# Kernel tuning notes

Measured on AMD Instinct MI355X. Metric: run time of the kernel, lower is better.

## Reference

```python
import jax, jax.numpy as jnp
import numpy as np

B, V, K, C = 32, 65536, 8, 3


def setup_inputs() -> dict:
    key = jax.random.key(0)
    k1, k2, k3, k4 = jax.random.split(key, 4)
    out = jax.random.normal(k1, (B, V, C), dtype=jnp.float32)
    tgt = jax.random.normal(k2, (B, V, C), dtype=jnp.float32)
    neighbor_idxs = jax.random.randint(k3, (V, K), 0, V, dtype=jnp.int32)
    # Laplacian weights: each row sums to -1 (lap = x - weighted mean of neighbors)
    w = jax.random.uniform(k4, (V, K), dtype=jnp.float32) + 1e-3
    neighbor_weights = -w / jnp.sum(w, axis=-1, keepdims=True)
    return {
        "out": out,
        "tgt": tgt,
        "neighbor_idxs": neighbor_idxs,
        "neighbor_weights": neighbor_weights,
    }


def _compute_laplacian(x, neighbor_idxs, neighbor_weights):
    # x: [B, V, C]; gather -> [B, V, K, C]; weighted sum over K; residual add
    gathered = x[:, neighbor_idxs]                       # [B, V, K, C]
    return x + jnp.sum(gathered * neighbor_weights[None, :, :, None], axis=2)


def reference(out, tgt, neighbor_idxs, neighbor_weights):
    lap_out = _compute_laplacian(out, neighbor_idxs, neighbor_weights)
    lap_tgt = _compute_laplacian(tgt, neighbor_idxs, neighbor_weights)
    return (lap_out - lap_tgt) ** 2
```

## Files before the change

### kernel.cpp

```cpp
#include <hip/hip_runtime.h>

#define BB 32
#define VV 65536
#define KK 8
#define CC 3

constexpr int TV   = 64;
constexpr int ROW  = BB * CC;
constexpr int PROW = ROW + 1;
constexpr int TILE_ELEMS = TV * ROW;
constexpr int ROWU = ROW / 2;

__device__ __forceinline__ unsigned int f2bf(float f) {
  unsigned int u = __float_as_uint(f);
  u += 0x7FFFu + ((u >> 16) & 1u);
  return u >> 16;
}
__device__ __forceinline__ float bflo(unsigned int u) { return __uint_as_float(u << 16); }
__device__ __forceinline__ float bfhi(unsigned int u) { return __uint_as_float(u & 0xFFFF0000u); }

__global__ __launch_bounds__(256) void lap_pass1_transpose_sub(
    const float* __restrict__ outp, const float* __restrict__ tgtp,
    unsigned int* __restrict__ dt) {
  __shared__ float tile[TV * PROW];
  const int t  = threadIdx.x;
  const int v0 = blockIdx.x * TV;

  const float4* o4 = (const float4*)outp;
  const float4* t4 = (const float4*)tgtp;
  const int src_base4 = (v0 * CC) >> 2;
  #pragma unroll
  for (int l4 = t; l4 < TILE_ELEMS / 4; l4 += 256) {
    int b  = l4 / (TV * CC / 4);
    int j4 = l4 - b * (TV * CC / 4);
    int src = b * (VV * CC / 4) + src_base4 + j4;
    float4 a = o4[src];
    float4 g = t4[src];
    float dv[4] = {a.x - g.x, a.y - g.y, a.z - g.z, a.w - g.w};
    int j = 4 * j4;
    #pragma unroll
    for (int q = 0; q < 4; q++) {
      int jj = j + q;
      int vrel = jj / CC, c = jj - vrel * CC;
      tile[vrel * PROW + b * CC + c] = dv[q];
    }
  }
  __syncthreads();

  uint4* dst = (uint4*)(dt + (size_t)v0 * ROWU);
  #pragma unroll
  for (int i8 = t; i8 < TILE_ELEMS / 8; i8 += 256) {
    int e = i8 * 8;
    int vrel = e / ROW, r = e - vrel * ROW;
    const float* p = &tile[vrel * PROW + r];
    uint4 o;
    o.x = f2bf(p[0]) | (f2bf(p[1]) << 16);
    o.y = f2bf(p[2]) | (f2bf(p[3]) << 16);
    o.z = f2bf(p[4]) | (f2bf(p[5]) << 16);
    o.w = f2bf(p[6]) | (f2bf(p[7]) << 16);
    dst[i8] = o;
  }
}

__global__ __launch_bounds__(256) void lap_pass2_gather(
    const unsigned int* __restrict__ dt, const int* __restrict__ nidx,
    const float* __restrict__ nw, float* __restrict__ res) {
  __shared__ float rtile[TV * PROW];
  __shared__ int   idx_s[TV * KK];
  __shared__ float w_s[TV * KK];
  const int t  = threadIdx.x;
  const int v0 = blockIdx.x * TV;

  for (int l = t; l < TV * KK; l += 256) {
    idx_s[l] = nidx[v0 * KK + l];
    w_s[l]   = nw[v0 * KK + l];
  }
  __syncthreads();

  const int g = t >> 4;
  const int l = t & 15;
  #pragma unroll 2
  for (int i = 0; i < TV / 16; i++) {
    const int vrel = i * 16 + g;
    const int v    = v0 + vrel;

    const int4*   ip = (const int4*)&idx_s[vrel * KK];
    const float4* wp = (const float4*)&w_s[vrel * KK];
    int4   ia = ip[0], ib = ip[1];
    float4 wa = wp[0], wb = wp[1];
    int   nbk[KK] = {ia.x, ia.y, ia.z, ia.w, ib.x, ib.y, ib.z, ib.w};
    float wk[KK]  = {wa.x, wa.y, wa.z, wa.w, wb.x, wb.y, wb.z, wb.w};

    const unsigned int* sp = dt + (size_t)v * ROWU + 3 * l;
    unsigned int s0 = sp[0], s1 = sp[1], s2 = sp[2];
    float x0 = bflo(s0), y0 = bfhi(s0), z0 = bflo(s1);
    float x1 = bfhi(s1), y1 = bflo(s2), z1 = bfhi(s2);

    #pragma unroll
    for (int k = 0; k < KK; k++) {
      const unsigned int* p = dt + (size_t)nbk[k] * ROWU + 3 * l;
      unsigned int u0 = p[0], u1 = p[1], u2 = p[2];
      const float wt = wk[k];
      x0 = fmaf(wt, bflo(u0), x0);
      y0 = fmaf(wt, bfhi(u0), y0);
      z0 = fmaf(wt, bflo(u1), z0);
      x1 = fmaf(wt, bfhi(u1), x1);
      y1 = fmaf(wt, bflo(u2), y1);
      z1 = fmaf(wt, bfhi(u2), z1);
    }
    float* rp = &rtile[vrel * PROW + 6 * l];
    rp[0] = x0 * x0; rp[1] = y0 * y0; rp[2] = z0 * z0;
    rp[3] = x1 * x1; rp[4] = y1 * y1; rp[5] = z1 * z1;
  }
  __syncthreads();

  float4* r4 = (float4*)res;
  const int dst_base4 = (v0 * CC) >> 2;
  #pragma unroll
  for (int l4 = t; l4 < TILE_ELEMS / 4; l4 += 256) {
    int b  = l4 / (TV * CC / 4);
    int j4 = l4 - b * (TV * CC / 4);
    int j  = 4 * j4;
    float tmp[4];
    #pragma unroll
    for (int q = 0; q < 4; q++) {
      int jj = j + q;
      int vrel = jj / CC, c = jj - vrel * CC;
      tmp[q] = rtile[vrel * PROW + b * CC + c];
    }
    r4[b * (VV * CC / 4) + dst_base4 + j4] = make_float4(tmp[0], tmp[1], tmp[2], tmp[3]);
  }
}

__global__ __launch_bounds__(256) void lap_fused_fallback(
    const float* __restrict__ outp, const float* __restrict__ tgtp,
    const int* __restrict__ nidx, const float* __restrict__ nw,
    float* __restrict__ res) {
  int tid = blockIdx.x * 256 + threadIdx.x;
  if (tid >= BB * VV) return;
  int v = tid & (VV - 1);
  int b = tid >> 16;
  float ax = 0.f, ay = 0.f, az = 0.f;
  #pragma unroll
  for (int k = 0; k < KK; k++) {
    int   nb = nidx[v * KK + k];
    float wt = nw[v * KK + k];
    const float* po = outp + ((size_t)b * VV + nb) * CC;
    const float* pt = tgtp + ((size_t)b * VV + nb) * CC;
    ax = fmaf(wt, po[0] - pt[0], ax);
    ay = fmaf(wt, po[1] - pt[1], ay);
    az = fmaf(wt, po[2] - pt[2], az);
  }
  const float* so = outp + (size_t)tid * CC;
  const float* st = tgtp + (size_t)tid * CC;
  float dx = so[0] - st[0] + ax;
  float dy = so[1] - st[1] + ay;
  float dz = so[2] - st[2] + az;
  float* rp = res + (size_t)tid * CC;
  rp[0] = dx * dx; rp[1] = dy * dy; rp[2] = dz * dz;
}

extern "C" void kernel_launch(void* const* d_in, const int* in_sizes, int n_in,
                              void* d_out, int out_size, void* d_ws, size_t ws_size,
                              hipStream_t stream) {
  const float* outp = (const float*)d_in[0];
  const float* tgtp = (const float*)d_in[1];
  const int*   nidx = (const int*)d_in[2];
  const float* nw   = (const float*)d_in[3];
  float* res = (float*)d_out;

  const size_t dt_bytes = (size_t)VV * ROW * 2;
  if (ws_size >= dt_bytes) {
    unsigned int* dt = (unsigned int*)d_ws;
    lap_pass1_transpose_sub<<<VV / TV, 256, 0, stream>>>(outp, tgtp, dt);
    lap_pass2_gather<<<VV / TV, 256, 0, stream>>>(dt, nidx, nw, res);
  } else {
    lap_fused_fallback<<<(BB * VV) / 256, 256, 0, stream>>>(outp, tgtp, nidx, nw, res);
  }
}
```

Baseline: 114.8 us.

## Fuse transpose and gather passes into one cooperative kernel with grid sync

```diff
diff --git a/kernel.cpp b/kernel.cpp
--- a/kernel.cpp
+++ b/kernel.cpp
@@ -1,4 +1,7 @@
 #include <hip/hip_runtime.h>
+#include <hip/hip_cooperative_groups.h>
+
+namespace cg = cooperative_groups;
 
 #define BB 32
 #define VV 65536
@@ -19,13 +22,11 @@
 __device__ __forceinline__ float bflo(unsigned int u) { return __uint_as_float(u << 16); }
 __device__ __forceinline__ float bfhi(unsigned int u) { return __uint_as_float(u & 0xFFFF0000u); }
 
-__global__ __launch_bounds__(256) void lap_pass1_transpose_sub(
-    const float* __restrict__ outp, const float* __restrict__ tgtp,
-    unsigned int* __restrict__ dt) {
-  __shared__ float tile[TV * PROW];
-  const int t  = threadIdx.x;
-  const int v0 = blockIdx.x * TV;
-
+struct U3 { unsigned int x, y, z; };
+
+__device__ __forceinline__ void do_transpose_sub(
+    const float* __restrict__ outp, const float* __restrict__ tgtp,
+    unsigned int* __restrict__ dt, float* tile, int v0, int t) {
   const float4* o4 = (const float4*)outp;
   const float4* t4 = (const float4*)tgtp;
   const int src_base4 = (v0 * CC) >> 2;
@@ -62,21 +63,10 @@
   }
 }
 
-__global__ __launch_bounds__(256) void lap_pass2_gather(
+__device__ __forceinline__ void do_gather(
     const unsigned int* __restrict__ dt, const int* __restrict__ nidx,
-    const float* __restrict__ nw, float* __restrict__ res) {
-  __shared__ float rtile[TV * PROW];
-  __shared__ int   idx_s[TV * KK];
-  __shared__ float w_s[TV * KK];
-  const int t  = threadIdx.x;
-  const int v0 = blockIdx.x * TV;
-
-  for (int l = t; l < TV * KK; l += 256) {
-    idx_s[l] = nidx[v0 * KK + l];
-    w_s[l]   = nw[v0 * KK + l];
-  }
-  __syncthreads();
-
+    const float* __restrict__ nw, float* __restrict__ res,
+    float* rtile, int v0, int t) {
   const int g = t >> 4;
   const int l = t & 15;
   #pragma unroll 2
@@ -84,29 +74,27 @@
     const int vrel = i * 16 + g;
     const int v    = v0 + vrel;
 
-    const int4*   ip = (const int4*)&idx_s[vrel * KK];
-    const float4* wp = (const float4*)&w_s[vrel * KK];
+    const int4*   ip = (const int4*)(nidx + (size_t)v * KK);
+    const float4* wp = (const float4*)(nw + (size_t)v * KK);
     int4   ia = ip[0], ib = ip[1];
     float4 wa = wp[0], wb = wp[1];
     int   nbk[KK] = {ia.x, ia.y, ia.z, ia.w, ib.x, ib.y, ib.z, ib.w};
     float wk[KK]  = {wa.x, wa.y, wa.z, wa.w, wb.x, wb.y, wb.z, wb.w};
 
-    const unsigned int* sp = dt + (size_t)v * ROWU + 3 * l;
-    unsigned int s0 = sp[0], s1 = sp[1], s2 = sp[2];
-    float x0 = bflo(s0), y0 = bfhi(s0), z0 = bflo(s1);
-    float x1 = bfhi(s1), y1 = bflo(s2), z1 = bfhi(s2);
+    U3 s = *(const U3*)(dt + (size_t)v * ROWU + 3 * l);
+    float x0 = bflo(s.x), y0 = bfhi(s.x), z0 = bflo(s.y);
+    float x1 = bfhi(s.y), y1 = bflo(s.z), z1 = bfhi(s.z);
 
     #pragma unroll
     for (int k = 0; k < KK; k++) {
-      const unsigned int* p = dt + (size_t)nbk[k] * ROWU + 3 * l;
-      unsigned int u0 = p[0], u1 = p[1], u2 = p[2];
+      U3 u = *(const U3*)(dt + (size_t)nbk[k] * ROWU + 3 * l);
       const float wt = wk[k];
-      x0 = fmaf(wt, bflo(u0), x0);
-      y0 = fmaf(wt, bfhi(u0), y0);
-      z0 = fmaf(wt, bflo(u1), z0);
-      x1 = fmaf(wt, bfhi(u1), x1);
-      y1 = fmaf(wt, bflo(u2), y1);
-      z1 = fmaf(wt, bfhi(u2), z1);
+      x0 = fmaf(wt, bflo(u.x), x0);
+      y0 = fmaf(wt, bfhi(u.x), y0);
+      z0 = fmaf(wt, bflo(u.y), z0);
+      x1 = fmaf(wt, bfhi(u.y), x1);
+      y1 = fmaf(wt, bflo(u.z), y1);
+      z1 = fmaf(wt, bfhi(u.z), z1);
     }
     float* rp = &rtile[vrel * PROW + 6 * l];
     rp[0] = x0 * x0; rp[1] = y0 * y0; rp[2] = z0 * z0;
@@ -132,6 +120,34 @@
   }
 }
 
+__global__ __launch_bounds__(256, 4) void lap_fused_coop(
+    const float* __restrict__ outp, const float* __restrict__ tgtp,
+    const int* __restrict__ nidx, const float* __restrict__ nw,
+    unsigned int* __restrict__ dt, float* __restrict__ res) {
+  __shared__ float smem[TV * PROW];
+  const int t  = threadIdx.x;
+  const int v0 = blockIdx.x * TV;
+
+  do_transpose_sub(outp, tgtp, dt, smem, v0, t);
+  __threadfence();
+  cg::this_grid().sync();
+  do_gather(dt, nidx, nw, res, smem, v0, t);
+}
+
+__global__ __launch_bounds__(256) void lap_pass1_transpose_sub(
+    const float* __restrict__ outp, const float* __restrict__ tgtp,
+    unsigned int* __restrict__ dt) {
+  __shared__ float tile[TV * PROW];
+  do_transpose_sub(outp, tgtp, dt, tile, blockIdx.x * TV, threadIdx.x);
+}
+
+__global__ __launch_bounds__(256) void lap_pass2_gather(
+    const unsigned int* __restrict__ dt, const int* __restrict__ nidx,
+    const float* __restrict__ nw, float* __restrict__ res) {
+  __shared__ float rtile[TV * PROW];
+  do_gather(dt, nidx, nw, res, rtile, blockIdx.x * TV, threadIdx.x);
+}
+
 __global__ __launch_bounds__(256) void lap_fused_fallback(
     const float* __restrict__ outp, const float* __restrict__ tgtp,
     const int* __restrict__ nidx, const float* __restrict__ nw,
@@ -172,6 +188,22 @@
   const size_t dt_bytes = (size_t)VV * ROW * 2;
   if (ws_size >= dt_bytes) {
     unsigned int* dt = (unsigned int*)d_ws;
+
+    static int coop = -1;
+    if (coop < 0) {
+      int nb = 0;
+      hipError_t e = hipOccupancyMaxActiveBlocksPerMultiprocessor(
+          &nb, lap_fused_coop, 256, 0);
+      coop = (e == hipSuccess && nb >= 4) ? 1 : 0;
+    }
+    if (coop == 1) {
+      void* params[] = {(void*)&outp, (void*)&tgtp, (void*)&nidx,
+                        (void*)&nw,   (void*)&dt,   (void*)&res};
+      hipError_t e = hipLaunchCooperativeKernel(
+          lap_fused_coop, dim3(VV / TV), dim3(256), params, 0u, stream);
+      if (e == hipSuccess) return;
+      coop = 0;
+    }
     lap_pass1_transpose_sub<<<VV / TV, 256, 0, stream>>>(outp, tgtp, dt);
     lap_pass2_gather<<<VV / TV, 256, 0, stream>>>(dt, nidx, nw, res);
   } else {
```

After: 112.1 us. 2.4% less time.

## Use nontemporal streaming loads/stores, halve vertex tile, read neighbor lists directly

Applied to the files above, without the earlier changes.

```diff
diff --git a/kernel.cpp b/kernel.cpp
--- a/kernel.cpp
+++ b/kernel.cpp
@@ -5,7 +5,7 @@
 #define KK 8
 #define CC 3
 
-constexpr int TV   = 64;
+constexpr int TV   = 32;
 constexpr int ROW  = BB * CC;
 constexpr int PROW = ROW + 1;
 constexpr int TILE_ELEMS = TV * ROW;
@@ -19,23 +19,33 @@
 __device__ __forceinline__ float bflo(unsigned int u) { return __uint_as_float(u << 16); }
 __device__ __forceinline__ float bfhi(unsigned int u) { return __uint_as_float(u & 0xFFFF0000u); }
 
-__global__ __launch_bounds__(256) void lap_pass1_transpose_sub(
+struct U3 { unsigned int x, y, z; };
+
+typedef float f4v __attribute__((ext_vector_type(4)));
+__device__ __forceinline__ float4 ldnt4(const float* p) {
+  f4v v = __builtin_nontemporal_load((const f4v*)p);
+  return make_float4(v[0], v[1], v[2], v[3]);
+}
+__device__ __forceinline__ void stnt4(float* p, float4 v) {
+  f4v x = {v.x, v.y, v.z, v.w};
+  __builtin_nontemporal_store(x, (f4v*)p);
+}
+
+__global__ __launch_bounds__(256, 8) void lap_pass1_transpose_sub(
     const float* __restrict__ outp, const float* __restrict__ tgtp,
     unsigned int* __restrict__ dt) {
   __shared__ float tile[TV * PROW];
   const int t  = threadIdx.x;
   const int v0 = blockIdx.x * TV;
 
-  const float4* o4 = (const float4*)outp;
-  const float4* t4 = (const float4*)tgtp;
   const int src_base4 = (v0 * CC) >> 2;
   #pragma unroll
   for (int l4 = t; l4 < TILE_ELEMS / 4; l4 += 256) {
     int b  = l4 / (TV * CC / 4);
     int j4 = l4 - b * (TV * CC / 4);
-    int src = b * (VV * CC / 4) + src_base4 + j4;
-    float4 a = o4[src];
-    float4 g = t4[src];
+    size_t src = (size_t)b * (VV * CC / 4) + src_base4 + j4;
+    float4 a = ldnt4(outp + 4 * src);
+    float4 g = ldnt4(tgtp + 4 * src);
     float dv[4] = {a.x - g.x, a.y - g.y, a.z - g.z, a.w - g.w};
     int j = 4 * j4;
     #pragma unroll
@@ -62,51 +72,41 @@
   }
 }
 
-__global__ __launch_bounds__(256) void lap_pass2_gather(
+__global__ __launch_bounds__(256, 8) void lap_pass2_gather(
     const unsigned int* __restrict__ dt, const int* __restrict__ nidx,
     const float* __restrict__ nw, float* __restrict__ res) {
   __shared__ float rtile[TV * PROW];
-  __shared__ int   idx_s[TV * KK];
-  __shared__ float w_s[TV * KK];
   const int t  = threadIdx.x;
   const int v0 = blockIdx.x * TV;
 
-  for (int l = t; l < TV * KK; l += 256) {
-    idx_s[l] = nidx[v0 * KK + l];
-    w_s[l]   = nw[v0 * KK + l];
-  }
-  __syncthreads();
-
   const int g = t >> 4;
   const int l = t & 15;
-  #pragma unroll 2
+  #pragma unroll
   for (int i = 0; i < TV / 16; i++) {
     const int vrel = i * 16 + g;
     const int v    = v0 + vrel;
 
-    const int4*   ip = (const int4*)&idx_s[vrel * KK];
-    const float4* wp = (const float4*)&w_s[vrel * KK];
+    const int4*   ip = (const int4*)(nidx + (size_t)v * KK);
+    const float4* wp = (const float4*)(nw + (size_t)v * KK);
     int4   ia = ip[0], ib = ip[1];
     float4 wa = wp[0], wb = wp[1];
     int   nbk[KK] = {ia.x, ia.y, ia.z, ia.w, ib.x, ib.y, ib.z, ib.w};
     float wk[KK]  = {wa.x, wa.y, wa.z, wa.w, wb.x, wb.y, wb.z, wb.w};
 
-    const unsigned int* sp = dt + (size_t)v * ROWU + 3 * l;
-    unsigned int s0 = sp[0], s1 = sp[1], s2 = sp[2];
-    float x0 = bflo(s0), y0 = bfhi(s0), z0 = bflo(s1);
-    float x1 = bfhi(s1), y1 = bflo(s2), z1 = bfhi(s2);
+    U3 s = *(const U3*)(dt + (size_t)v * ROWU + 3 * l);
+    float x0 = bflo(s.x), y0 = bfhi(s.x), z0 = bflo(s.y);
+    float x1 = bfhi(s.y), y1 = bflo(s.z), z1 = bfhi(s.z);
 
     #pragma unroll
     for (int k = 0; k < KK; k++) {
-      const unsigned int* p = dt + (size_t)nbk[k] * ROWU + 3 * l;
-      unsigned int u0 = p[0], u1 = p[1], u2 = p[2];
+      U3 u = *(const U3*)(dt + (size_t)nbk[k] * ROWU + 3 * l);
       const float wt = wk[k];
-      x0 = fmaf(wt, bflo(u0), x0);
-      y0 = fmaf(wt, bfhi(u0), y0);
-      z0 = fmaf(wt, bflo(u1), z0);
-      x1 = fmaf(wt, bfhi(u1), x1);
-      y1 = fmaf(wt, bflo(u2), y1);
-      z1 = fmaf(wt, bfhi(u2), z1);
+      x0 = fmaf(wt, bflo(u.x), x0);
+      y0 = fmaf(wt, bfhi(u.x), y0);
+      z0 = fmaf(wt, bflo(u.y), z0);
+      x1 = fmaf(wt, bfhi(u.y), x1);
+      y1 = fmaf(wt, bflo(u.z), y1);
+      z1 = fmaf(wt, bfhi(u.z), z1);
     }
     float* rp = &rtile[vrel * PROW + 6 * l];
     rp[0] = x0 * x0; rp[1] = y0 * y0; rp[2] = z0 * z0;
@@ -114,7 +114,6 @@
   }
   __syncthreads();
 
-  float4* r4 = (float4*)res;
   const int dst_base4 = (v0 * CC) >> 2;
   #pragma unroll
   for (int l4 = t; l4 < TILE_ELEMS / 4; l4 += 256) {
@@ -128,7 +127,8 @@
       int vrel = jj / CC, c = jj - vrel * CC;
       tmp[q] = rtile[vrel * PROW + b * CC + c];
     }
-    r4[b * (VV * CC / 4) + dst_base4 + j4] = make_float4(tmp[0], tmp[1], tmp[2], tmp[3]);
+    stnt4(res + 4 * ((size_t)b * (VV * CC / 4) + dst_base4 + j4),
+          make_float4(tmp[0], tmp[1], tmp[2], tmp[3]));
   }
 }
 
```

After: 128.9 us. 1.12x slower.

## Encode difference vectors as shared-exponent 8-bit triplets to shrink gather traffic

Applied to the files above, without the earlier changes.

```diff
diff --git a/kernel.cpp b/kernel.cpp
--- a/kernel.cpp
+++ b/kernel.cpp
@@ -9,17 +9,36 @@
 constexpr int ROW  = BB * CC;
 constexpr int PROW = ROW + 1;
 constexpr int TILE_ELEMS = TV * ROW;
-constexpr int ROWU = ROW / 2;
-
-__device__ __forceinline__ unsigned int f2bf(float f) {
-  unsigned int u = __float_as_uint(f);
-  u += 0x7FFFu + ((u >> 16) & 1u);
-  return u >> 16;
-}
-__device__ __forceinline__ float bflo(unsigned int u) { return __uint_as_float(u << 16); }
-__device__ __forceinline__ float bfhi(unsigned int u) { return __uint_as_float(u & 0xFFFF0000u); }
-
-__global__ __launch_bounds__(256) void lap_pass1_transpose_sub(
+constexpr int RDW  = BB;
+
+__device__ __forceinline__ unsigned int enc3(float x0, float x1, float x2) {
+  float a0 = fabsf(x0), a1 = fabsf(x1), a2 = fabsf(x2);
+  float A  = fmaxf(a0, fmaxf(a1, a2));
+  if (A == 0.f) return 0u;
+  int ex;
+  (void)frexpf(A, &ex);
+  int e5 = ex + 15;
+  e5 = e5 < 0 ? 0 : (e5 > 31 ? 31 : e5);
+  float s = ldexpf(1.f, 23 - e5);
+  unsigned m0 = (unsigned)fminf(fmaf(a0, s, 0.5f), 255.f);
+  unsigned m1 = (unsigned)fminf(fmaf(a1, s, 0.5f), 255.f);
+  unsigned m2 = (unsigned)fminf(fmaf(a2, s, 0.5f), 255.f);
+  unsigned s0 = __float_as_uint(x0) >> 31;
+  unsigned s1 = __float_as_uint(x1) >> 31;
+  unsigned s2 = __float_as_uint(x2) >> 31;
+  return ((unsigned)e5 << 27) | (s2 << 26) | (m2 << 18)
+       | (s1 << 17) | (m1 << 9) | (s0 << 8) | m0;
+}
+__device__ __forceinline__ void dec3(unsigned int u,
+                                     float& v0, float& v1, float& v2) {
+  float sc  = ldexpf(1.f, (int)(u >> 27) - 23);
+  float nsc = -sc;
+  v0 = (float)(u & 255u)         * (((u >> 8)  & 1u) ? nsc : sc);
+  v1 = (float)((u >> 9) & 255u)  * (((u >> 17) & 1u) ? nsc : sc);
+  v2 = (float)((u >> 18) & 255u) * (((u >> 26) & 1u) ? nsc : sc);
+}
+
+__global__ __launch_bounds__(256) void lap_pass1_encode(
     const float* __restrict__ outp, const float* __restrict__ tgtp,
     unsigned int* __restrict__ dt) {
   __shared__ float tile[TV * PROW];
@@ -47,18 +66,19 @@
   }
   __syncthreads();
 
-  uint4* dst = (uint4*)(dt + (size_t)v0 * ROWU);
-  #pragma unroll
-  for (int i8 = t; i8 < TILE_ELEMS / 8; i8 += 256) {
-    int e = i8 * 8;
-    int vrel = e / ROW, r = e - vrel * ROW;
-    const float* p = &tile[vrel * PROW + r];
-    uint4 o;
-    o.x = f2bf(p[0]) | (f2bf(p[1]) << 16);
-    o.y = f2bf(p[2]) | (f2bf(p[3]) << 16);
-    o.z = f2bf(p[4]) | (f2bf(p[5]) << 16);
-    o.w = f2bf(p[6]) | (f2bf(p[7]) << 16);
-    dst[i8] = o;
+  uint4* dst = (uint4*)(dt + (size_t)v0 * RDW);
+  #pragma unroll
+  for (int u = t; u < TV * BB / 4; u += 256) {
+    int vrel = u >> 3;
+    int b0   = (u & 7) * 4;
+    unsigned int w[4];
+    #pragma unroll
+    for (int q = 0; q < 4; q++) {
+      const float* p = &tile[vrel * PROW + (b0 + q) * CC];
+      w[q] = enc3(p[0], p[1], p[2]);
+    }
+    uint4 o; o.x = w[0]; o.y = w[1]; o.z = w[2]; o.w = w[3];
+    dst[u] = o;
   }
 }
 
@@ -71,10 +91,8 @@
   const int t  = threadIdx.x;
   const int v0 = blockIdx.x * TV;
 
-  for (int l = t; l < TV * KK; l += 256) {
-    idx_s[l] = nidx[v0 * KK + l];
-    w_s[l]   = nw[v0 * KK + l];
-  }
+  ((int2*)idx_s)[t]  = ((const int2*)(nidx + (size_t)v0 * KK))[t];
+  ((float2*)w_s)[t]  = ((const float2*)(nw + (size_t)v0 * KK))[t];
   __syncthreads();
 
   const int g = t >> 4;
@@ -91,22 +109,24 @@
     int   nbk[KK] = {ia.x, ia.y, ia.z, ia.w, ib.x, ib.y, ib.z, ib.w};
     float wk[KK]  = {wa.x, wa.y, wa.z, wa.w, wb.x, wb.y, wb.z, wb.w};
 
-    const unsigned int* sp = dt + (size_t)v * ROWU + 3 * l;
-    unsigned int s0 = sp[0], s1 = sp[1], s2 = sp[2];
-    float x0 = bflo(s0), y0 = bfhi(s0), z0 = bflo(s1);
-    float x1 = bfhi(s1), y1 = bflo(s2), z1 = bfhi(s2);
+    uint2 su = *(const uint2*)(dt + (size_t)v * RDW + 2 * l);
+    float x0, y0, z0, x1, y1, z1;
+    dec3(su.x, x0, y0, z0);
+    dec3(su.y, x1, y1, z1);
 
     #pragma unroll
     for (int k = 0; k < KK; k++) {
-      const unsigned int* p = dt + (size_t)nbk[k] * ROWU + 3 * l;
-      unsigned int u0 = p[0], u1 = p[1], u2 = p[2];
+      uint2 u2 = *(const uint2*)(dt + (size_t)nbk[k] * RDW + 2 * l);
       const float wt = wk[k];
-      x0 = fmaf(wt, bflo(u0), x0);
-      y0 = fmaf(wt, bfhi(u0), y0);
-      z0 = fmaf(wt, bflo(u1), z0);
-      x1 = fmaf(wt, bfhi(u1), x1);
-      y1 = fmaf(wt, bflo(u2), y1);
-      z1 = fmaf(wt, bfhi(u2), z1);
+      float p0, p1, p2, p3, p4, p5;
+      dec3(u2.x, p0, p1, p2);
+      dec3(u2.y, p3, p4, p5);
+      x0 = fmaf(wt, p0, x0);
+      y0 = fmaf(wt, p1, y0);
+      z0 = fmaf(wt, p2, z0);
+      x1 = fmaf(wt, p3, x1);
+      y1 = fmaf(wt, p4, y1);
+      z1 = fmaf(wt, p5, z1);
     }
     float* rp = &rtile[vrel * PROW + 6 * l];
     rp[0] = x0 * x0; rp[1] = y0 * y0; rp[2] = z0 * z0;
@@ -169,10 +189,10 @@
   const float* nw   = (const float*)d_in[3];
   float* res = (float*)d_out;
 
-  const size_t dt_bytes = (size_t)VV * ROW * 2;
+  const size_t dt_bytes = (size_t)VV * RDW * 4;
   if (ws_size >= dt_bytes) {
     unsigned int* dt = (unsigned int*)d_ws;
-    lap_pass1_transpose_sub<<<VV / TV, 256, 0, stream>>>(outp, tgtp, dt);
+    lap_pass1_encode<<<VV / TV, 256, 0, stream>>>(outp, tgtp, dt);
     lap_pass2_gather<<<VV / TV, 256, 0, stream>>>(dt, nidx, nw, res);
   } else {
     lap_fused_fallback<<<(BB * VV) / 256, 256, 0, stream>>>(outp, tgtp, nidx, nw, res);
```

New measurement: 111.9 us. -2.6%, faster.
